# Performance work log

Measured on AMD Instinct MI355X. Metric: run time of the kernel, lower is better.

Reference implementation:

```python
import jax, jax.numpy as jnp
import numpy as np

N = 20000
E = 320000
IN_DIM = 128
HID = 64
HEADS = 8
OUT_DIM = 128
NEG_SLOPE = 0.2  # PyG GATConv default leaky_relu slope


def _glorot(key, shape):
    fan_in = shape[0] if len(shape) > 1 else shape[-1]
    return jax.random.normal(key, shape, dtype=jnp.float32) / jnp.sqrt(jnp.float32(fan_in))


def setup_inputs() -> dict:
    key = jax.random.key(0)
    ks = jax.random.split(key, 16)
    x = jax.random.normal(ks[0], (N, IN_DIM), dtype=jnp.float32)
    edge_index = jax.random.randint(ks[1], (2, E), 0, N, dtype=jnp.int32)
    HC = HEADS * HID
    return {
        "x": x,
        "edge_index": edge_index,
        # layer 1: in -> heads*hid (concat)
        "W1": _glorot(ks[2], (IN_DIM, HC)),
        "a_src1": _glorot(ks[3], (HEADS, HID)),
        "a_dst1": _glorot(ks[4], (HEADS, HID)),
        "b1": jnp.zeros((HC,), jnp.float32),
        # layer 2: heads*hid -> heads*hid (concat)
        "W2": _glorot(ks[5], (HC, HC)),
        "a_src2": _glorot(ks[6], (HEADS, HID)),
        "a_dst2": _glorot(ks[7], (HEADS, HID)),
        "b2": jnp.zeros((HC,), jnp.float32),
        # layer 3: heads*hid -> out, heads=1, concat=False
        "W3": _glorot(ks[8], (HC, OUT_DIM)),
        "a_src3": _glorot(ks[9], (1, OUT_DIM)),
        "a_dst3": _glorot(ks[10], (1, OUT_DIM)),
        "b3": jnp.zeros((OUT_DIM,), jnp.float32),
    }


def _gat_layer(x, src, dst, W, a_src, a_dst, b, heads, concat):
    # x: [N, F_in] -> h: [N, H, C]
    n = x.shape[0]
    h = (x @ W).reshape(n, heads, -1)
    # per-node attention half-logits: [N, H]
    al_src = jnp.sum(h * a_src[None], axis=-1)
    al_dst = jnp.sum(h * a_dst[None], axis=-1)
    # per-edge logits with leaky relu: [E, H]
    e = jax.nn.leaky_relu(al_src[src] + al_dst[dst], NEG_SLOPE)
    # segment softmax over incoming edges of each dst node
    emax = jax.ops.segment_max(e, dst, num_segments=n)
    ex = jnp.exp(e - emax[dst])
    den = jax.ops.segment_sum(ex, dst, num_segments=n)
    alpha = ex / (den[dst] + 1e-16)
    # weighted scatter-aggregate of source features: [E, H, C] -> [N, H, C]
    out = jax.ops.segment_sum(h[src] * alpha[:, :, None], dst, num_segments=n)
    out = out.reshape(n, -1) if concat else out.mean(axis=1)
    return out + b


def reference(x, edge_index, W1, a_src1, a_dst1, b1, W2, a_src2, a_dst2, b2,
              W3, a_src3, a_dst3, b3):
    # PyG GATConv adds self-loops by default
    loops = jnp.arange(N, dtype=edge_index.dtype)
    src = jnp.concatenate([edge_index[0], loops])
    dst = jnp.concatenate([edge_index[1], loops])
    # eval mode: dropout is identity
    h = _gat_layer(x, src, dst, W1, a_src1, a_dst1, b1, HEADS, True)
    h = jax.nn.elu(h)
    h = _gat_layer(h, src, dst, W2, a_src2, a_dst2, b2, HEADS, True)
    h = jax.nn.elu(h)
    out = _gat_layer(h, src, dst, W3, a_src3, a_dst3, b3, 1, False)
    return out
```

## Files before the change

### kernel.cpp

```cpp
#include <hip/hip_runtime.h>
#include <math.h>

#define NN 20000
#define EE 320000
#define ETOT 340000
#define NHEADS 8
#define HID 64
#define HCV 512
#define IND 128
#define OUTD 128
#define NEG_SLOPE 0.2f

typedef __attribute__((ext_vector_type(8))) _Float16 half8;
typedef __attribute__((ext_vector_type(4))) float floatx4;

__device__ __forceinline__ void cvt_one(const float* W, _Float16* T, int idx, int K, int N) {
    int k = idx / N, n = idx - k * N;
    T[(size_t)n * K + k] = (_Float16)W[idx];
}

#define S1 (IND * HCV)
#define S2 (HCV * HCV)
#define S3 (HCV * OUTD)
#define STOT (S1 + S2 + S3)
#define XTOT (NN * IND)
__global__ void prep_kernel(const float* __restrict__ W1, const float* __restrict__ W2,
                            const float* __restrict__ W3, const float* __restrict__ x,
                            const float* __restrict__ as1, const float* __restrict__ ad1,
                            _Float16* __restrict__ T1, _Float16* __restrict__ T2,
                            _Float16* __restrict__ T3, _Float16* __restrict__ xh,
                            float* __restrict__ w1p, int* __restrict__ cnt) {
    int idx = blockIdx.x * blockDim.x + threadIdx.x;
    if (idx < S1) cvt_one(W1, T1, idx, IND, HCV);
    else if (idx < S1 + S2) cvt_one(W2, T2, idx - S1, HCV, HCV);
    else if (idx < STOT) cvt_one(W3, T3, idx - S1 - S2, HCV, OUTD);
    else if (idx < STOT + NN) cnt[idx - STOT] = 0;
    else if (idx < STOT + NN + XTOT) {
        int j = idx - STOT - NN;
        xh[j] = (_Float16)x[j];
    } else if (idx < STOT + NN + XTOT + IND * 16) {
        int j = idx - STOT - NN - XTOT;
        int c = j >> 4, o = j & 15;
        int hh = o & 7;
        const float* av = (o < 8) ? as1 : ad1;
        float s = 0.f;
        #pragma unroll 8
        for (int jj = 0; jj < HID; jj++)
            s = fmaf(W1[c * HCV + hh * HID + jj], av[hh * HID + jj], s);
        w1p[c * 16 + o] = s;
    }
}


__global__ void count_kernel(const int* __restrict__ ei, int* __restrict__ cnt) {
    int i = blockIdx.x * blockDim.x + threadIdx.x;
    if (i >= ETOT) return;
    int v = (i < EE) ? ei[EE + i] : (i - EE);
    atomicAdd(&cnt[v], 1);
}

#define SCH 20
__global__ __launch_bounds__(1024) void scan_kernel(const int* __restrict__ cnt,
                                                    int* __restrict__ row_ptr,
                                                    int* __restrict__ cursor) {
    __shared__ int wtot[16];
    __shared__ int woff[16];
    int t = threadIdx.x;
    int lane = t & 63;
    int wid = t >> 6;
    int base = t * SCH;
    int vals[SCH];
    int s = 0;
    #pragma unroll
    for (int i = 0; i < SCH; i++) {
        int idx = base + i;
        int v = (idx < NN) ? cnt[idx] : 0;
        vals[i] = v;
        s += v;
    }
    int incl = s;
    #pragma unroll
    for (int off = 1; off < 64; off <<= 1) {
        int u = __shfl_up(incl, off);
        if (lane >= off) incl += u;
    }
    int excl = incl - s;
    if (lane == 63) wtot[wid] = incl;
    __syncthreads();
    if (t == 0) {
        int run = 0;
        #pragma unroll
        for (int j = 0; j < 16; j++) { woff[j] = run; run += wtot[j]; }
        row_ptr[NN] = run;
    }
    __syncthreads();
    int run = woff[wid] + excl;
    #pragma unroll
    for (int i = 0; i < SCH; i++) {
        int idx = base + i;
        if (idx < NN) { row_ptr[idx] = run; cursor[idx] = run; run += vals[i]; }
    }
}

__global__ void fill_kernel(const int* __restrict__ ei, int* __restrict__ cursor,
                            int* __restrict__ csr_src) {
    int i = blockIdx.x * blockDim.x + threadIdx.x;
    if (i >= ETOT) return;
    int u, v;
    if (i < EE) { u = ei[i]; v = ei[EE + i]; }
    else        { u = i - EE; v = i - EE; }
    int pos = atomicAdd(&cursor[v], 1);
    csr_src[pos] = u;
}

__global__ void al1_thin(const float* __restrict__ x, const float* __restrict__ w1p,
                         float* __restrict__ als, float* __restrict__ ald) {
    int gid = blockIdx.x * blockDim.x + threadIdx.x;
    int node = gid >> 4, o = gid & 15;
    if (node >= NN) return;
    const float* xr = x + (size_t)node * IND;
    float s = 0.f;
    #pragma unroll 4
    for (int c = 0; c < IND; c++)
        s = fmaf(xr[c], w1p[c * 16 + o], s);
    if (o < 8) als[node * 8 + o] = s;
    else       ald[node * 8 + (o - 8)] = s;
}

__global__ __launch_bounds__(256) void gather1_kernel(const _Float16* __restrict__ xh,
                                                      const int* __restrict__ row_ptr,
                                                      const int* __restrict__ csr_src,
                                                      const float* __restrict__ als,
                                                      const float* __restrict__ ald,
                                                      _Float16* __restrict__ xagg) {
    int lane = threadIdx.x & 63;
    int v = blockIdx.x * 4 + (threadIdx.x >> 6);
    if (v >= NN) return;
    int hd = lane >> 3;
    int cg = lane & 7;
    float adst = ald[v * NHEADS + hd];
    int s0 = row_ptr[v], s1 = row_ptr[v + 1];
    float acc[16] = {};
    float l = 0.f;
    int i = s0;
    for (; i + 4 <= s1; i += 4) {
        int u[4]; float p[4];
        #pragma unroll
        for (int e = 0; e < 4; e++) u[e] = csr_src[i + e];
        #pragma unroll
        for (int e = 0; e < 4; e++) {
            float t = als[u[e] * NHEADS + hd] + adst;
            t = (t > 0.f) ? t : NEG_SLOPE * t;
            p[e] = __expf(fminf(t, 80.f));
        }
        half8 a[4], b[4];
        #pragma unroll
        for (int e = 0; e < 4; e++) {
            a[e] = *(const half8*)&xh[(size_t)u[e] * IND + cg * 16];
            b[e] = *(const half8*)&xh[(size_t)u[e] * IND + cg * 16 + 8];
        }
        #pragma unroll
        for (int e = 0; e < 4; e++) {
            l += p[e];
            #pragma unroll
            for (int j = 0; j < 8; j++) {
                acc[j]     = fmaf(p[e], (float)a[e][j], acc[j]);
                acc[j + 8] = fmaf(p[e], (float)b[e][j], acc[j + 8]);
            }
        }
    }
    for (; i < s1; i++) {
        int u0 = csr_src[i];
        float t0 = als[u0 * NHEADS + hd] + adst;
        t0 = (t0 > 0.f) ? t0 : NEG_SLOPE * t0;
        float p0 = __expf(fminf(t0, 80.f));
        half8 a0 = *(const half8*)&xh[(size_t)u0 * IND + cg * 16];
        half8 b0 = *(const half8*)&xh[(size_t)u0 * IND + cg * 16 + 8];
        l += p0;
        #pragma unroll
        for (int j = 0; j < 8; j++) {
            acc[j]     = fmaf(p0, (float)a0[j], acc[j]);
            acc[j + 8] = fmaf(p0, (float)b0[j], acc[j + 8]);
        }
    }
    float inv = 1.f / (l + 1e-16f);
    half8 o0, o1;
    #pragma unroll
    for (int j = 0; j < 8; j++) {
        o0[j] = (_Float16)(acc[j] * inv);
        o1[j] = (_Float16)(acc[j + 8] * inv);
    }
    size_t base = (size_t)v * (NHEADS * IND) + hd * IND + cg * 16;
    *(half8*)&xagg[base] = o0;
    *(half8*)&xagg[base + 8] = o1;
}

#define LDK 40
__global__ __launch_bounds__(256) void gemm1_bd(const _Float16* __restrict__ xagg,
                                                const _Float16* __restrict__ Bt,
                                                const float* __restrict__ bias,
                                                _Float16* __restrict__ gact,
                                                int M) {
    __shared__ _Float16 sA[64 * LDK];
    __shared__ _Float16 sB[64 * LDK];
    int tid = threadIdx.x;
    int lane = tid & 63;
    int wv = tid >> 6;
    int m0 = blockIdx.x * 64;
    int h = blockIdx.y;
    int quad = lane >> 4;
    int l15 = lane & 15;
    int arow = tid >> 2;
    int ac4 = tid & 3;

    floatx4 acc[4] = {};

    for (int k0 = 0; k0 < IND; k0 += 32) {
        {
            int gm = m0 + arow;
            int4 va;
            if (gm < M) va = *(const int4*)&xagg[(size_t)gm * (NHEADS * IND) + h * IND + k0 + ac4 * 8];
            else        va = make_int4(0, 0, 0, 0);
            *(int4*)&sA[arow * LDK + ac4 * 8] = va;
            int gn = h * 64 + arow;
            int4 vb = *(const int4*)&Bt[(size_t)gn * IND + k0 + ac4 * 8];
            *(int4*)&sB[arow * LDK + ac4 * 8] = vb;
        }
        __syncthreads();
        half8 a[4], b;
        #pragma unroll
        for (int i = 0; i < 4; i++)
            a[i] = *(const half8*)&sA[(i * 16 + l15) * LDK + quad * 8];
        b = *(const half8*)&sB[(wv * 16 + l15) * LDK + quad * 8];
        #pragma unroll
        for (int i = 0; i < 4; i++)
            acc[i] = __builtin_amdgcn_mfma_f32_16x16x32_f16(a[i], b, acc[i], 0, 0, 0);
        __syncthreads();
    }
    #pragma unroll
    for (int i = 0; i < 4; i++) {
        #pragma unroll
        for (int r = 0; r < 4; r++) {
            int gm = m0 + i * 16 + quad * 4 + r;
            if (gm < M) {
                int col = h * 64 + wv * 16 + l15;
                float o = acc[i][r] + bias[col];
                o = (o > 0.f) ? o : (__expf(o) - 1.f);
                gact[(size_t)gm * HCV + col] = (_Float16)o;
            }
        }
    }
}

__global__ __launch_bounds__(256) void gemm_l2(const _Float16* __restrict__ A,
                                               const _Float16* __restrict__ Bt,
                                               _Float16* __restrict__ C16,
                                               const float* __restrict__ a_src,
                                               const float* __restrict__ a_dst,
                                               float* __restrict__ als,
                                               float* __restrict__ ald,
                                               int M, int K) {
    __shared__ _Float16 sA[64 * LDK];
    __shared__ _Float16 sB[128 * LDK];
    __shared__ float psum_s[4][64];
    __shared__ float psum_d[4][64];
    int tid = threadIdx.x;
    int lane = tid & 63;
    int wv = tid >> 6;
    int m0 = blockIdx.x * 64, n0 = blockIdx.y * 128;
    int quad = lane >> 4;
    int l15 = lane & 15;
    int arow = tid >> 2;
    int ac4 = tid & 3;

    floatx4 acc[4][2] = {};

    for (int k0 = 0; k0 < K; k0 += 32) {
        {
            int gm = m0 + arow;
            int4 va;
            if (gm < M) va = *(const int4*)&A[(size_t)gm * K + k0 + ac4 * 8];
            else        va = make_int4(0, 0, 0, 0);
            *(int4*)&sA[arow * LDK + ac4 * 8] = va;
            #pragma unroll
            for (int r = 0; r < 2; r++) {
                int gn = n0 + arow + r * 64;
                int4 vb = *(const int4*)&Bt[(size_t)gn * K + k0 + ac4 * 8];
                *(int4*)&sB[(arow + r * 64) * LDK + ac4 * 8] = vb;
            }
        }
        __syncthreads();
        half8 a[4], b[2];
        #pragma unroll
        for (int i = 0; i < 4; i++)
            a[i] = *(const half8*)&sA[(i * 16 + l15) * LDK + quad * 8];
        #pragma unroll
        for (int j = 0; j < 2; j++)
            b[j] = *(const half8*)&sB[(wv * 32 + j * 16 + l15) * LDK + quad * 8];
        #pragma unroll
        for (int i = 0; i < 4; i++)
            #pragma unroll
            for (int j = 0; j < 2; j++)
                acc[i][j] = __builtin_amdgcn_mfma_f32_16x16x32_f16(a[i], b[j], acc[i][j], 0, 0, 0);
        __syncthreads();
    }
    #pragma unroll
    for (int i = 0; i < 4; i++) {
        #pragma unroll
        for (int r = 0; r < 4; r++) {
            int gm = m0 + i * 16 + quad * 4 + r;
            if (gm < M) {
                #pragma unroll
                for (int j = 0; j < 2; j++)
                    C16[(size_t)gm * HCV + n0 + wv * 32 + j * 16 + l15] = (_Float16)acc[i][j][r];
            }
        }
    }
    int h0 = n0 >> 6;
    float as_v[2], ad_v[2];
    #pragma unroll
    for (int j = 0; j < 2; j++) {
        int dim = (wv * 32 + j * 16 + l15) & 63;
        int hh = h0 + (wv >> 1);
        as_v[j] = a_src[hh * HID + dim];
        ad_v[j] = a_dst[hh * HID + dim];
    }
    #pragma unroll
    for (int i = 0; i < 4; i++) {
        #pragma unroll
        for (int r = 0; r < 4; r++) {
            float ps = acc[i][0][r] * as_v[0] + acc[i][1][r] * as_v[1];
            float pd = acc[i][0][r] * ad_v[0] + acc[i][1][r] * ad_v[1];
            #pragma unroll
            for (int off = 1; off <= 8; off <<= 1) {
                ps += __shfl_xor(ps, off);
                pd += __shfl_xor(pd, off);
            }
            if (l15 == 0) {
                int row = i * 16 + quad * 4 + r;
                psum_s[wv][row] = ps;
                psum_d[wv][row] = pd;
            }
        }
    }
    __syncthreads();
    if (tid < 64) {
        int gm = m0 + tid;
        if (gm < M) {
            als[gm * NHEADS + h0]     = psum_s[0][tid] + psum_s[1][tid];
            als[gm * NHEADS + h0 + 1] = psum_s[2][tid] + psum_s[3][tid];
            ald[gm * NHEADS + h0]     = psum_d[0][tid] + psum_d[1][tid];
            ald[gm * NHEADS + h0 + 1] = psum_d[2][tid] + psum_d[3][tid];
        }
    }
}

__global__ __launch_bounds__(256) void gemm3(const _Float16* __restrict__ A,
                                             const _Float16* __restrict__ Bt,
                                             _Float16* __restrict__ C16,
                                             const float* __restrict__ a_src,
                                             const float* __restrict__ a_dst,
                                             float* __restrict__ als,
                                             float* __restrict__ ald,
                                             int M, int K) {
    __shared__ _Float16 sA[64 * LDK];
    __shared__ _Float16 sB[128 * LDK];
    __shared__ float psum_s[4][64];
    __shared__ float psum_d[4][64];
    int tid = threadIdx.x;
    int lane = tid & 63;
    int wv = tid >> 6;
    int m0 = blockIdx.x * 64;
    int quad = lane >> 4;
    int l15 = lane & 15;
    int arow = tid >> 2;
    int ac4 = tid & 3;

    floatx4 acc[4][2] = {};

    for (int k0 = 0; k0 < K; k0 += 32) {
        {
            int gm = m0 + arow;
            int4 va;
            if (gm < M) va = *(const int4*)&A[(size_t)gm * K + k0 + ac4 * 8];
            else        va = make_int4(0, 0, 0, 0);
            *(int4*)&sA[arow * LDK + ac4 * 8] = va;
            #pragma unroll
            for (int r = 0; r < 2; r++) {
                int gn = arow + r * 64;
                int4 vb = *(const int4*)&Bt[(size_t)gn * K + k0 + ac4 * 8];
                *(int4*)&sB[(arow + r * 64) * LDK + ac4 * 8] = vb;
            }
        }
        __syncthreads();
        half8 a[4], b[2];
        #pragma unroll
        for (int i = 0; i < 4; i++)
            a[i] = *(const half8*)&sA[(i * 16 + l15) * LDK + quad * 8];
        #pragma unroll
        for (int j = 0; j < 2; j++)
            b[j] = *(const half8*)&sB[(wv * 32 + j * 16 + l15) * LDK + quad * 8];
        #pragma unroll
        for (int i = 0; i < 4; i++)
            #pragma unroll
            for (int j = 0; j < 2; j++)
                acc[i][j] = __builtin_amdgcn_mfma_f32_16x16x32_f16(a[i], b[j], acc[i][j], 0, 0, 0);
        __syncthreads();
    }
    #pragma unroll
    for (int i = 0; i < 4; i++) {
        #pragma unroll
        for (int r = 0; r < 4; r++) {
            int gm = m0 + i * 16 + quad * 4 + r;
            if (gm < M) {
                #pragma unroll
                for (int j = 0; j < 2; j++)
                    C16[(size_t)gm * OUTD + wv * 32 + j * 16 + l15] = (_Float16)acc[i][j][r];
            }
        }
    }
    float as_v[2], ad_v[2];
    #pragma unroll
    for (int j = 0; j < 2; j++) {
        as_v[j] = a_src[wv * 32 + j * 16 + l15];
        ad_v[j] = a_dst[wv * 32 + j * 16 + l15];
    }
    #pragma unroll
    for (int i = 0; i < 4; i++) {
        #pragma unroll
        for (int r = 0; r < 4; r++) {
            float ps = acc[i][0][r] * as_v[0] + acc[i][1][r] * as_v[1];
            float pd = acc[i][0][r] * ad_v[0] + acc[i][1][r] * ad_v[1];
            #pragma unroll
            for (int off = 1; off <= 8; off <<= 1) {
                ps += __shfl_xor(ps, off);
                pd += __shfl_xor(pd, off);
            }
            if (l15 == 0) {
                int row = i * 16 + quad * 4 + r;
                psum_s[wv][row] = ps;
                psum_d[wv][row] = pd;
            }
        }
    }
    __syncthreads();
    if (tid < 64) {
        int gm = m0 + tid;
        if (gm < M) {
            als[gm] = psum_s[0][tid] + psum_s[1][tid] + psum_s[2][tid] + psum_s[3][tid];
            ald[gm] = psum_d[0][tid] + psum_d[1][tid] + psum_d[2][tid] + psum_d[3][tid];
        }
    }
}

__global__ __launch_bounds__(256) void gather2_kernel(const _Float16* __restrict__ h,
                                                      const int* __restrict__ row_ptr,
                                                      const int* __restrict__ csr_src,
                                                      const float* __restrict__ als,
                                                      const float* __restrict__ ald,
                                                      const float* __restrict__ bias,
                                                      _Float16* __restrict__ gout) {
    int lane = threadIdx.x & 63;
    int v = blockIdx.x * 4 + (threadIdx.x >> 6);
    if (v >= NN) return;
    int hd = lane >> 3;
    float adst = ald[v * NHEADS + hd];
    int s0 = row_ptr[v], s1 = row_ptr[v + 1];
    float acc[8] = {};
    float l = 0.f;
    int i = s0;
    for (; i + 8 <= s1; i += 8) {
        int u[8]; float p[8];
        #pragma unroll
        for (int e = 0; e < 8; e++) u[e] = csr_src[i + e];
        #pragma unroll
        for (int e = 0; e < 8; e++) {
            float t = als[u[e] * NHEADS + hd] + adst;
            t = (t > 0.f) ? t : NEG_SLOPE * t;
            p[e] = __expf(fminf(t, 80.f));
        }
        half8 xv[8];
        #pragma unroll
        for (int e = 0; e < 8; e++)
            xv[e] = *(const half8*)&h[(size_t)u[e] * HCV + lane * 8];
        #pragma unroll
        for (int e = 0; e < 8; e++) {
            l += p[e];
            #pragma unroll
            for (int j = 0; j < 8; j++)
                acc[j] = fmaf(p[e], (float)xv[e][j], acc[j]);
        }
    }
    for (; i + 2 <= s1; i += 2) {
        int u0 = csr_src[i], u1 = csr_src[i + 1];
        float t0 = als[u0 * NHEADS + hd] + adst;
        float t1 = als[u1 * NHEADS + hd] + adst;
        t0 = (t0 > 0.f) ? t0 : NEG_SLOPE * t0;
        t1 = (t1 > 0.f) ? t1 : NEG_SLOPE * t1;
        float p0 = __expf(fminf(t0, 80.f));
        float p1 = __expf(fminf(t1, 80.f));
        half8 x0 = *(const half8*)&h[(size_t)u0 * HCV + lane * 8];
        half8 x1 = *(const half8*)&h[(size_t)u1 * HCV + lane * 8];
        l += p0 + p1;
        #pragma unroll
        for (int j = 0; j < 8; j++) {
            acc[j] = fmaf(p0, (float)x0[j], acc[j]);
            acc[j] = fmaf(p1, (float)x1[j], acc[j]);
        }
    }
    if (i < s1) {
        int u0 = csr_src[i];
        float t0 = als[u0 * NHEADS + hd] + adst;
        t0 = (t0 > 0.f) ? t0 : NEG_SLOPE * t0;
        float p0 = __expf(fminf(t0, 80.f));
        half8 x0 = *(const half8*)&h[(size_t)u0 * HCV + lane * 8];
        l += p0;
        #pragma unroll
        for (int j = 0; j < 8; j++)
            acc[j] = fmaf(p0, (float)x0[j], acc[j]);
    }
    float inv = 1.f / (l + 1e-16f);
    half8 hv;
    #pragma unroll
    for (int j = 0; j < 8; j++) {
        float o = fmaf(acc[j], inv, bias[lane * 8 + j]);
        o = (o > 0.f) ? o : (__expf(o) - 1.f);
        hv[j] = (_Float16)o;
    }
    *(half8*)&gout[(size_t)v * HCV + lane * 8] = hv;
}

__global__ __launch_bounds__(256) void gather3_kernel(const _Float16* __restrict__ h,
                                                      const int* __restrict__ row_ptr,
                                                      const int* __restrict__ csr_src,
                                                      const float* __restrict__ als,
                                                      const float* __restrict__ ald,
                                                      const float* __restrict__ bias,
                                                      float* __restrict__ out) {
    int lane = threadIdx.x & 63;
    int v = blockIdx.x * 4 + (threadIdx.x >> 6);
    if (v >= NN) return;
    int e_sub = lane >> 4;
    int cg = lane & 15;
    float adst = ald[v];
    int s0 = row_ptr[v], s1 = row_ptr[v + 1];
    float m = -INFINITY;
    for (int i = s0 + e_sub; i < s1; i += 4) {
        int u = csr_src[i];
        float t = als[u] + adst;
        t = (t > 0.f) ? t : NEG_SLOPE * t;
        m = fmaxf(m, t);
    }
    m = fmaxf(m, __shfl_xor(m, 16));
    m = fmaxf(m, __shfl_xor(m, 32));
    float acc[8] = {};
    float l = 0.f;
    for (int i = s0 + e_sub; i < s1; i += 4) {
        int u = csr_src[i];
        float t = als[u] + adst;
        t = (t > 0.f) ? t : NEG_SLOPE * t;
        float p = __expf(t - m);
        half8 x = *(const half8*)&h[(size_t)u * OUTD + cg * 8];
        l += p;
        #pragma unroll
        for (int j = 0; j < 8; j++)
            acc[j] = fmaf(p, (float)x[j], acc[j]);
    }
    l += __shfl_xor(l, 16);
    l += __shfl_xor(l, 32);
    #pragma unroll
    for (int j = 0; j < 8; j++) {
        acc[j] += __shfl_xor(acc[j], 16);
        acc[j] += __shfl_xor(acc[j], 32);
    }
    if (e_sub == 0) {
        float inv = 1.f / (l + 1e-16f);
        float4 o0, o1;
        o0.x = fmaf(acc[0], inv, bias[cg * 8 + 0]);
        o0.y = fmaf(acc[1], inv, bias[cg * 8 + 1]);
        o0.z = fmaf(acc[2], inv, bias[cg * 8 + 2]);
        o0.w = fmaf(acc[3], inv, bias[cg * 8 + 3]);
        o1.x = fmaf(acc[4], inv, bias[cg * 8 + 4]);
        o1.y = fmaf(acc[5], inv, bias[cg * 8 + 5]);
        o1.z = fmaf(acc[6], inv, bias[cg * 8 + 6]);
        o1.w = fmaf(acc[7], inv, bias[cg * 8 + 7]);
        *(float4*)&out[(size_t)v * OUTD + cg * 8] = o0;
        *(float4*)&out[(size_t)v * OUTD + cg * 8 + 4] = o1;
    }
}


extern "C" void kernel_launch(void* const* d_in, const int* in_sizes, int n_in,
                              void* d_out, int out_size, void* d_ws, size_t ws_size,
                              hipStream_t stream) {
    const float* x     = (const float*)d_in[0];
    const int*   ei    = (const int*)d_in[1];
    const float* W1    = (const float*)d_in[2];
    const float* as1   = (const float*)d_in[3];
    const float* ad1   = (const float*)d_in[4];
    const float* b1    = (const float*)d_in[5];
    const float* W2    = (const float*)d_in[6];
    const float* as2   = (const float*)d_in[7];
    const float* ad2   = (const float*)d_in[8];
    const float* b2    = (const float*)d_in[9];
    const float* W3    = (const float*)d_in[10];
    const float* as3   = (const float*)d_in[11];
    const float* ad3   = (const float*)d_in[12];
    const float* b3    = (const float*)d_in[13];
    float* out = (float*)d_out;

    size_t off = 0;
    auto carve = [&](size_t bytes) {
        void* p = (char*)d_ws + off;
        off += (bytes + 255) & ~(size_t)255;
        return p;
    };
    int* row_ptr   = (int*)carve((NN + 1) * sizeof(int));
    int* cursor    = (int*)carve(NN * sizeof(int));
    int* csr_src   = (int*)carve(ETOT * sizeof(int));
    _Float16* xh   = (_Float16*)carve((size_t)NN * IND * sizeof(_Float16));
    _Float16* xagg = (_Float16*)carve((size_t)NN * NHEADS * IND * sizeof(_Float16));
    _Float16* gact = (_Float16*)carve((size_t)NN * HCV * sizeof(_Float16));
    _Float16* hf16 = (_Float16*)carve((size_t)NN * HCV * sizeof(_Float16));
    _Float16* h3   = (_Float16*)carve((size_t)NN * OUTD * sizeof(_Float16));
    float* als     = (float*)carve((size_t)NN * NHEADS * sizeof(float));
    float* ald     = (float*)carve((size_t)NN * NHEADS * sizeof(float));
    float* w1p     = (float*)carve((size_t)IND * 16 * sizeof(float));
    _Float16* W1T  = (_Float16*)carve((size_t)S1 * sizeof(_Float16));
    _Float16* W2T  = (_Float16*)carve((size_t)S2 * sizeof(_Float16));
    _Float16* W3T  = (_Float16*)carve((size_t)S3 * sizeof(_Float16));
    _Float16* gact2 = xagg;
    (void)ws_size; (void)n_in; (void)in_sizes; (void)out_size;

    dim3 blk(256);

    int prep_n = STOT + NN + XTOT + IND * 16;
    prep_kernel<<<(prep_n + 255) / 256, blk, 0, stream>>>(W1, W2, W3, x, as1, ad1,
        W1T, W2T, W3T, xh, w1p, cursor);

    count_kernel<<<(ETOT + 255) / 256, blk, 0, stream>>>(ei, cursor);
    scan_kernel<<<1, 1024, 0, stream>>>(cursor, row_ptr, cursor);
    fill_kernel<<<(ETOT + 255) / 256, blk, 0, stream>>>(ei, cursor, csr_src);

    int mt64 = (NN + 63) / 64;
    int nwaves_n = (NN + 3) / 4;

    al1_thin<<<(NN * 16 + 255) / 256, blk, 0, stream>>>(x, w1p, als, ald);
    gather1_kernel<<<nwaves_n, blk, 0, stream>>>(xh, row_ptr, csr_src, als, ald, xagg);
    gemm1_bd<<<dim3(mt64, NHEADS), blk, 0, stream>>>(xagg, W1T, b1, gact, NN);

    gemm_l2<<<dim3(mt64, HCV / 128), blk, 0, stream>>>(gact, W2T, hf16, as2, ad2, als, ald, NN, HCV);
    gather2_kernel<<<nwaves_n, blk, 0, stream>>>(hf16, row_ptr, csr_src, als, ald, b2, gact2);

    gemm3<<<dim3(mt64, 1), blk, 0, stream>>>(gact2, W3T, h3, as3, ad3, als, ald, NN, HCV);
    gather3_kernel<<<nwaves_n, blk, 0, stream>>>(h3, row_ptr, csr_src, als, ald, b3, out);
}
```

Before: 341.6 us.

## Split layer-2 attention into alpha precompute and channel-chunked gather kernel

Adds a separate kernel that computes per-edge softmax weights (with max subtraction) in fp16 plus per-node inverse denominators. The layer-2 gather then reads these precomputed weights and splits the 512 channels into four 128-channel chunks across blocks, so each wave loads half2 per lane instead of half8. Blocks are interleaved so chunks of the same node group run close together, aiming for more parallelism and better L2 locality on the feature gather. In exchange it adds an extra launch, an edge-by-head weight buffer to write and read, and four-fold re-reads of the CSR index array.

```diff
diff --git a/kernel.cpp b/kernel.cpp
--- a/kernel.cpp
+++ b/kernel.cpp
@@ -12,6 +12,7 @@
 #define NEG_SLOPE 0.2f
 
 typedef __attribute__((ext_vector_type(8))) _Float16 half8;
+typedef __attribute__((ext_vector_type(2))) _Float16 half2v;
 typedef __attribute__((ext_vector_type(4))) float floatx4;
 
 __device__ __forceinline__ void cvt_one(const float* W, _Float16* T, int idx, int K, int N) {
@@ -453,81 +454,94 @@
     }
 }
 
+__global__ __launch_bounds__(256) void alpha2_kernel(const int* __restrict__ row_ptr,
+                                                     const int* __restrict__ csr_src,
+                                                     const float* __restrict__ als,
+                                                     const float* __restrict__ ald,
+                                                     _Float16* __restrict__ pT,
+                                                     float* __restrict__ invden) {
+    int lane = threadIdx.x & 63;
+    int v = blockIdx.x * 4 + (threadIdx.x >> 6);
+    if (v >= NN) return;
+    int e_sub = lane >> 3;
+    int hd = lane & 7;
+    float adst = ald[v * NHEADS + hd];
+    int s0 = row_ptr[v], s1 = row_ptr[v + 1];
+    float m = -INFINITY;
+    for (int base = s0; base < s1; base += 8) {
+        int i = base + e_sub;
+        if (i < s1) {
+            int u = csr_src[i];
+            float t = als[u * NHEADS + hd] + adst;
+            t = (t > 0.f) ? t : NEG_SLOPE * t;
+            m = fmaxf(m, t);
+        }
+    }
+    #pragma unroll
+    for (int off = 8; off <= 32; off <<= 1) m = fmaxf(m, __shfl_xor(m, off));
+    float l = 0.f;
+    for (int base = s0; base < s1; base += 8) {
+        int i = base + e_sub;
+        if (i < s1) {
+            int u = csr_src[i];
+            float t = als[u * NHEADS + hd] + adst;
+            t = (t > 0.f) ? t : NEG_SLOPE * t;
+            _Float16 ph = (_Float16)__expf(t - m);
+            pT[(size_t)i * 8 + hd] = ph;
+            l += (float)ph;
+        }
+    }
+    #pragma unroll
+    for (int off = 8; off <= 32; off <<= 1) l += __shfl_xor(l, off);
+    if (e_sub == 0) invden[v * NHEADS + hd] = 1.f / (l + 1e-16f);
+}
+
 __global__ __launch_bounds__(256) void gather2_kernel(const _Float16* __restrict__ h,
                                                       const int* __restrict__ row_ptr,
                                                       const int* __restrict__ csr_src,
-                                                      const float* __restrict__ als,
-                                                      const float* __restrict__ ald,
+                                                      const _Float16* __restrict__ pT,
+                                                      const float* __restrict__ invden,
                                                       const float* __restrict__ bias,
                                                       _Float16* __restrict__ gout) {
+    int g = blockIdx.x & 7;
+    int chunk = g >> 1;
+    int ngrp = (blockIdx.x >> 3) * 2 + (g & 1);
+    int wv = threadIdx.x >> 6;
     int lane = threadIdx.x & 63;
-    int v = blockIdx.x * 4 + (threadIdx.x >> 6);
-    if (v >= NN) return;
-    int hd = lane >> 3;
-    float adst = ald[v * NHEADS + hd];
+    int v = ngrp * 4 + wv;
+    int ch = chunk * 128 + lane * 2;
+    int hd = ch >> 6;
     int s0 = row_ptr[v], s1 = row_ptr[v + 1];
-    float acc[8] = {};
-    float l = 0.f;
+    float a0 = 0.f, a1 = 0.f;
     int i = s0;
     for (; i + 8 <= s1; i += 8) {
-        int u[8]; float p[8];
+        int u[8]; float p[8]; half2v xv[8];
         #pragma unroll
         for (int e = 0; e < 8; e++) u[e] = csr_src[i + e];
         #pragma unroll
+        for (int e = 0; e < 8; e++) p[e] = (float)pT[(size_t)(i + e) * 8 + hd];
+        #pragma unroll
+        for (int e = 0; e < 8; e++) xv[e] = *(const half2v*)&h[(size_t)u[e] * HCV + ch];
+        #pragma unroll
         for (int e = 0; e < 8; e++) {
-            float t = als[u[e] * NHEADS + hd] + adst;
-            t = (t > 0.f) ? t : NEG_SLOPE * t;
-            p[e] = __expf(fminf(t, 80.f));
-        }
-        half8 xv[8];
-        #pragma unroll
-        for (int e = 0; e < 8; e++)
-            xv[e] = *(const half8*)&h[(size_t)u[e] * HCV + lane * 8];
-        #pragma unroll
-        for (int e = 0; e < 8; e++) {
-            l += p[e];
-            #pragma unroll
-            for (int j = 0; j < 8; j++)
-                acc[j] = fmaf(p[e], (float)xv[e][j], acc[j]);
-        }
-    }
-    for (; i + 2 <= s1; i += 2) {
-        int u0 = csr_src[i], u1 = csr_src[i + 1];
-        float t0 = als[u0 * NHEADS + hd] + adst;
-        float t1 = als[u1 * NHEADS + hd] + adst;
-        t0 = (t0 > 0.f) ? t0 : NEG_SLOPE * t0;
-        t1 = (t1 > 0.f) ? t1 : NEG_SLOPE * t1;
-        float p0 = __expf(fminf(t0, 80.f));
-        float p1 = __expf(fminf(t1, 80.f));
-        half8 x0 = *(const half8*)&h[(size_t)u0 * HCV + lane * 8];
-        half8 x1 = *(const half8*)&h[(size_t)u1 * HCV + lane * 8];
-        l += p0 + p1;
-        #pragma unroll
-        for (int j = 0; j < 8; j++) {
-            acc[j] = fmaf(p0, (float)x0[j], acc[j]);
-            acc[j] = fmaf(p1, (float)x1[j], acc[j]);
-        }
-    }
-    if (i < s1) {
+            a0 = fmaf(p[e], (float)xv[e][0], a0);
+            a1 = fmaf(p[e], (float)xv[e][1], a1);
+        }
+    }
+    for (; i < s1; i++) {
         int u0 = csr_src[i];
-        float t0 = als[u0 * NHEADS + hd] + adst;
-        t0 = (t0 > 0.f) ? t0 : NEG_SLOPE * t0;
-        float p0 = __expf(fminf(t0, 80.f));
-        half8 x0 = *(const half8*)&h[(size_t)u0 * HCV + lane * 8];
-        l += p0;
-        #pragma unroll
-        for (int j = 0; j < 8; j++)
-            acc[j] = fmaf(p0, (float)x0[j], acc[j]);
-    }
-    float inv = 1.f / (l + 1e-16f);
-    half8 hv;
-    #pragma unroll
-    for (int j = 0; j < 8; j++) {
-        float o = fmaf(acc[j], inv, bias[lane * 8 + j]);
-        o = (o > 0.f) ? o : (__expf(o) - 1.f);
-        hv[j] = (_Float16)o;
-    }
-    *(half8*)&gout[(size_t)v * HCV + lane * 8] = hv;
+        float p0 = (float)pT[(size_t)i * 8 + hd];
+        half2v x0 = *(const half2v*)&h[(size_t)u0 * HCV + ch];
+        a0 = fmaf(p0, (float)x0[0], a0);
+        a1 = fmaf(p0, (float)x0[1], a1);
+    }
+    float inv = invden[v * NHEADS + hd];
+    float o0 = fmaf(a0, inv, bias[ch]);
+    float o1 = fmaf(a1, inv, bias[ch + 1]);
+    o0 = (o0 > 0.f) ? o0 : (__expf(o0) - 1.f);
+    o1 = (o1 > 0.f) ? o1 : (__expf(o1) - 1.f);
+    half2v o; o[0] = (_Float16)o0; o[1] = (_Float16)o1;
+    *(half2v*)&gout[(size_t)v * HCV + ch] = o;
 }
 
 __global__ __launch_bounds__(256) void gather3_kernel(const _Float16* __restrict__ h,
@@ -625,6 +639,8 @@
     _Float16* h3   = (_Float16*)carve((size_t)NN * OUTD * sizeof(_Float16));
     float* als     = (float*)carve((size_t)NN * NHEADS * sizeof(float));
     float* ald     = (float*)carve((size_t)NN * NHEADS * sizeof(float));
+    float* invden  = (float*)carve((size_t)NN * NHEADS * sizeof(float));
+    _Float16* pT   = (_Float16*)carve((size_t)ETOT * NHEADS * sizeof(_Float16));
     float* w1p     = (float*)carve((size_t)IND * 16 * sizeof(float));
     _Float16* W1T  = (_Float16*)carve((size_t)S1 * sizeof(_Float16));
     _Float16* W2T  = (_Float16*)carve((size_t)S2 * sizeof(_Float16));
@@ -650,7 +666,8 @@
     gemm1_bd<<<dim3(mt64, NHEADS), blk, 0, stream>>>(xagg, W1T, b1, gact, NN);
 
     gemm_l2<<<dim3(mt64, HCV / 128), blk, 0, stream>>>(gact, W2T, hf16, as2, ad2, als, ald, NN, HCV);
-    gather2_kernel<<<nwaves_n, blk, 0, stream>>>(hf16, row_ptr, csr_src, als, ald, b2, gact2);
+    alpha2_kernel<<<nwaves_n, blk, 0, stream>>>(row_ptr, csr_src, als, ald, pT, invden);
+    gather2_kernel<<<NN, blk, 0, stream>>>(hf16, row_ptr, csr_src, pT, invden, b2, gact2);
 
     gemm3<<<dim3(mt64, 1), blk, 0, stream>>>(gact2, W3T, h3, as3, ad3, als, ald, NN, HCV);
     gather3_kernel<<<nwaves_n, blk, 0, stream>>>(h3, row_ptr, csr_src, als, ald, b3, out);
```

Result: slower. 360.3 us (+5.5%).
